# Performance work log

Measured on AMD Instinct MI355X. Metric: run time of the kernel, lower is better.

## Reference

```python
import jax, jax.numpy as jnp
import numpy as np
from jax import lax

DN = ('NCHW', 'OIHW', 'NCHW')


def conv2d(x, w, b, stride, pad):
    y = lax.conv_general_dilated(x, w, (stride, stride), [(pad, pad), (pad, pad)],
                                 dimension_numbers=DN)
    return y + b[None, :, None, None]


def conv_transpose2d_k4s2p1(x, w, b):
    # torch ConvTranspose2d(k=4, s=2, p=1); w is torch layout [Cin, Cout, 4, 4].
    # Equivalent forward conv: lhs_dilation=2, pad = k-1-p = 2, spatially-flipped kernel.
    k = jnp.flip(w, (2, 3)).transpose(1, 0, 2, 3)  # -> OIHW [Cout, Cin, 4, 4]
    y = lax.conv_general_dilated(x, k, (1, 1), [(2, 2), (2, 2)],
                                 lhs_dilation=(2, 2), dimension_numbers=DN)
    return y + b[None, :, None, None]


def setup_inputs() -> dict:
    key = jax.random.key(0)
    ks = jax.random.split(key, 16)

    def w(k, shape):
        fan_in = int(np.prod(shape[1:]))
        return jax.random.normal(k, shape, jnp.float32) * np.float32(1.0 / np.sqrt(fan_in))

    inp = {}
    inp['x'] = jax.random.uniform(ks[0], (256, 1, 128, 128), jnp.float32)
    # Encoder
    inp['enc_w1'] = w(ks[1], (32, 1, 4, 4));   inp['enc_b1'] = jnp.zeros((32,), jnp.float32)
    inp['enc_w2'] = w(ks[2], (64, 32, 4, 4));  inp['enc_b2'] = jnp.zeros((64,), jnp.float32)
    inp['enc_w3'] = w(ks[3], (64, 64, 3, 3));  inp['enc_b3'] = jnp.zeros((64,), jnp.float32)
    inp['enc_w4'] = w(ks[4], (32, 64, 1, 1));  inp['enc_b4'] = jnp.zeros((32,), jnp.float32)
    # Codebook: uniform(-sqrt(3/512), sqrt(3/512))
    mx = np.float32(np.sqrt(3.0 / 512.0))
    inp['codebook'] = jax.random.uniform(ks[5], (512, 32), jnp.float32, -mx, mx)
    # Decoder
    inp['dec_w1'] = w(ks[6], (64, 32, 3, 3));  inp['dec_b1'] = jnp.zeros((64,), jnp.float32)
    inp['dect_w1'] = w(ks[7], (64, 32, 4, 4)); inp['dect_b1'] = jnp.zeros((32,), jnp.float32)  # torch [Cin,Cout,k,k]
    inp['dect_w2'] = w(ks[8], (32, 1, 4, 4));  inp['dect_b2'] = jnp.zeros((1,), jnp.float32)
    return inp


def vqvae_forward(x, enc_w1, enc_b1, enc_w2, enc_b2, enc_w3, enc_b3, enc_w4, enc_b4,
                  codebook, dec_w1, dec_b1, dect_w1, dect_b1, dect_w2, dect_b2):
    # Encoder: 128 -> 64 -> 32 spatial, 32 channels out
    h = jax.nn.relu(conv2d(x, enc_w1, enc_b1, 2, 1))
    h = jax.nn.relu(conv2d(h, enc_w2, enc_b2, 2, 1))
    h = jax.nn.relu(conv2d(h, enc_w3, enc_b3, 1, 1))
    z = conv2d(h, enc_w4, enc_b4, 1, 0)            # [B, 32, 32, 32]

    # Vector quantization (NCHW -> NHWC -> flat)
    zin = jnp.moveaxis(z, 1, -1)                   # [B, H, W, D]
    flat = zin.reshape(-1, zin.shape[-1])          # [N, D]
    dists = (jnp.sum(flat * flat, -1, keepdims=True)
             + jnp.sum(codebook * codebook, -1)
             - 2.0 * flat @ codebook.T)            # [N, K]
    idx = jnp.argmin(dists, -1)                    # [N]
    quant = codebook[idx].reshape(zin.shape)       # == one_hot @ codebook

    emb_loss = jnp.mean((quant - lax.stop_gradient(zin)) ** 2)
    com_loss = 0.26 * jnp.mean((lax.stop_gradient(quant) - zin) ** 2)
    vq_loss = emb_loss + com_loss
    quant = zin + lax.stop_gradient(quant - zin)   # straight-through
    qz = jnp.moveaxis(quant, -1, 1)                # [B, 32, 32, 32]

    # Decoder: 32 -> 64 -> 128 spatial
    d = jax.nn.relu(conv2d(qz, dec_w1, dec_b1, 1, 1))
    d = jax.nn.relu(conv_transpose2d_k4s2p1(d, dect_w1, dect_b1))
    recon = jax.nn.sigmoid(conv_transpose2d_k4s2p1(d, dect_w2, dect_b2))
    return recon, vq_loss


def reference(x, enc_w1, enc_b1, enc_w2, enc_b2, enc_w3, enc_b3, enc_w4, enc_b4,
              codebook, dec_w1, dec_b1, dect_w1, dect_b1, dect_w2, dect_b2):
    return vqvae_forward(x, enc_w1, enc_b1, enc_w2, enc_b2, enc_w3, enc_b3, enc_w4, enc_b4,
                         codebook, dec_w1, dec_b1, dect_w1, dect_b1, dect_w2, dect_b2)
```

## Files before the change

kernel.cpp:

```cpp
#include <hip/hip_runtime.h>
#include <math.h>

typedef __attribute__((ext_vector_type(8))) short short8;
typedef __attribute__((ext_vector_type(4))) float f32x4;

__device__ inline unsigned short f2bf(float f) {
  unsigned u = __float_as_uint(f);
  u = (u + 0x7fffu + ((u >> 16) & 1u)) >> 16;
  return (unsigned short)u;
}

__global__ __launch_bounds__(256, 4)
void conv1_lds(const float* __restrict__ x, const float* __restrict__ w,
               const float* __restrict__ bias, float* __restrict__ out) {
  int bid = blockIdx.x;
  int cchunk = bid & 1;
  int t4 = (bid >> 1) & 3;
  int n = bid >> 3;
  int co0 = cchunk * 16;
  int y0 = t4 * 16;
  int yi0 = 2 * y0 - 1;

  __shared__ float xs[34 * 128];
  __shared__ float wl[16][16];

  int t = threadIdx.x;
  for (int idx = t; idx < 34 * 128; idx += 256) {
    int gy = yi0 + (idx >> 7);
    int gx = idx & 127;
    bool ok = (unsigned)gy < 128;
    xs[idx] = ok ? x[(size_t)n * 16384 + gy * 128 + gx] : 0.f;
  }
  {
    int cc = t & 15;
    int tap = t >> 4;
    if (t < 256) wl[tap][cc] = w[(size_t)(co0 + cc) * 16 + tap];
  }
  __syncthreads();

  int sx = t & 63;
  int rg = t >> 6;

  float acc[4][16];
#pragma unroll
  for (int j = 0; j < 4; j++)
#pragma unroll
    for (int c = 0; c < 16; c++) acc[j][c] = 0.f;

  int ix0 = 2 * sx - 1;
#pragma unroll
  for (int ky = 0; ky < 4; ky++) {
#pragma unroll
    for (int kx = 0; kx < 4; kx++) {
      int ix = ix0 + kx;
      bool xok = (unsigned)ix < 128;
      float xv[4];
#pragma unroll
      for (int j = 0; j < 4; j++) {
        int lrow = 2 * (4 * rg + j) + ky;
        float v = xs[lrow * 128 + (xok ? ix : 0)];
        xv[j] = xok ? v : 0.f;
      }
      const float* wr = &wl[ky * 4 + kx][0];
#pragma unroll
      for (int c = 0; c < 16; c += 4) {
        float4 wv = *(const float4*)(wr + c);
#pragma unroll
        for (int j = 0; j < 4; j++) {
          acc[j][c + 0] = fmaf(xv[j], wv.x, acc[j][c + 0]);
          acc[j][c + 1] = fmaf(xv[j], wv.y, acc[j][c + 1]);
          acc[j][c + 2] = fmaf(xv[j], wv.z, acc[j][c + 2]);
          acc[j][c + 3] = fmaf(xv[j], wv.w, acc[j][c + 3]);
        }
      }
    }
  }

#pragma unroll
  for (int j = 0; j < 4; j++) {
    int oy = y0 + 4 * rg + j;
    float* op = out + (((size_t)n * 32 + co0) * 64 + oy) * 64 + sx;
#pragma unroll
    for (int c = 0; c < 16; c++) {
      float v = acc[j][c] + bias[co0 + c];
      op[(size_t)c * 4096] = fmaxf(v, 0.f);
    }
  }
}

template<int CIN, int COUT, int CCH>
__global__ __launch_bounds__(256, 4)
void conv4x4s2_h4(const float* __restrict__ x, const float* __restrict__ w,
                  const float* __restrict__ bias, float* __restrict__ out) {
  constexpr int NCH = COUT / CCH;
  int bid = blockIdx.x;
  int cchunk = bid % NCH;
  int n = bid / NCH;
  int co0 = cchunk * CCH;

  __shared__ float xs[66 * 64];
  __shared__ float wl[16][CCH];

  int t = threadIdx.x;
  int sx = t & 31;
  int sy0 = t >> 5;
  int ix0 = 2 * sx - 1;

  if (t < 128) {
    int r = (t >> 6) ? 65 : 0;
    xs[r * 64 + (t & 63)] = 0.f;
  }

  float acc[4][CCH];
#pragma unroll
  for (int j = 0; j < 4; j++)
#pragma unroll
    for (int c = 0; c < CCH; c++) acc[j][c] = 0.f;

  const float* xn = x + (size_t)n * CIN * 4096;

  for (int ci = 0; ci < CIN; ci++) {
    __syncthreads();
#pragma unroll
    for (int k = 0; k < 4; k++) {
      int idx = k * 1024 + t * 4;
      int row = idx >> 6;
      int col = idx & 63;
      *(float4*)(xs + (row + 1) * 64 + col) =
          *(const float4*)(xn + (size_t)ci * 4096 + idx);
    }
    {
      int cc = t & (CCH - 1);
      int tap = t >> 4;
      if (tap < 16) wl[tap][cc] = w[(size_t)(co0 + cc) * (CIN * 16) + ci * 16 + tap];
    }
    __syncthreads();

#pragma unroll
    for (int ky = 0; ky < 4; ky++) {
#pragma unroll
      for (int kx = 0; kx < 4; kx++) {
        int ix = ix0 + kx;
        bool xok = (unsigned)ix < 64;
        int ixs = xok ? ix : 0;
        float xv[4];
#pragma unroll
        for (int j = 0; j < 4; j++) {
          int row = 2 * (sy0 + j * 8) + ky;
          float v = xs[row * 64 + ixs];
          xv[j] = xok ? v : 0.f;
        }
        const float* wr = &wl[ky * 4 + kx][0];
#pragma unroll
        for (int c = 0; c < CCH; c += 4) {
          float4 wv = *(const float4*)(wr + c);
#pragma unroll
          for (int j = 0; j < 4; j++) {
            acc[j][c + 0] = fmaf(xv[j], wv.x, acc[j][c + 0]);
            acc[j][c + 1] = fmaf(xv[j], wv.y, acc[j][c + 1]);
            acc[j][c + 2] = fmaf(xv[j], wv.z, acc[j][c + 2]);
            acc[j][c + 3] = fmaf(xv[j], wv.w, acc[j][c + 3]);
          }
        }
      }
    }
  }

#pragma unroll
  for (int j = 0; j < 4; j++) {
    int sy = sy0 + j * 8;
    float* op = out + (((size_t)n * COUT + co0) * 32 + sy) * 32 + sx;
#pragma unroll
    for (int c = 0; c < CCH; c++) {
      float v = acc[j][c] + bias[co0 + c];
      v = fmaxf(v, 0.f);
      op[(size_t)c * 1024] = v;
    }
  }
}

template<int CIN, int COUT, int CCH>
__global__ __launch_bounds__(256, 4)
void conv3x3_h4(const float* __restrict__ x, const float* __restrict__ w,
                const float* __restrict__ bias, float* __restrict__ out) {
  constexpr int NCH = COUT / CCH;
  int bid = blockIdx.x;
  int cchunk = bid % NCH;
  int n = bid / NCH;
  int co0 = cchunk * CCH;

  __shared__ float xs[4][34 * 32];
  __shared__ float wl[4 * 9][CCH];

  int t = threadIdx.x;
  int sx = t & 31;
  int rg = t >> 5;

  {
    int p = t >> 6;
    int idx = t & 63;
    int row = (idx >> 5) ? 33 : 0;
    xs[p][row * 32 + (idx & 31)] = 0.f;
  }

  float acc[4][CCH];
#pragma unroll
  for (int j = 0; j < 4; j++)
#pragma unroll
    for (int c = 0; c < CCH; c++) acc[j][c] = 0.f;

  const float* xn = x + (size_t)n * CIN * 1024;

  for (int cg = 0; cg < CIN / 4; cg++) {
    __syncthreads();
#pragma unroll
    for (int k = 0; k < 4; k++) {
      int row = t >> 3;
      int col = (t & 7) * 4;
      *(float4*)(&xs[k][(row + 1) * 32 + col]) =
          *(const float4*)(xn + (size_t)(cg * 4 + k) * 1024 + t * 4);
    }
    for (int i = t; i < 4 * 9 * CCH; i += 256) {
      int cc = i % CCH;
      int row = i / CCH;
      int c4 = row / 9, kk = row % 9;
      wl[row][cc] = w[(size_t)(co0 + cc) * (CIN * 9) + (cg * 4 + c4) * 9 + kk];
    }
    __syncthreads();

#pragma unroll
    for (int c4 = 0; c4 < 4; c4++) {
      const float* xc = &xs[c4][0];
      float xv[6][3];
#pragma unroll
      for (int cx = 0; cx < 3; cx++) {
        int ix = sx - 1 + cx;
        bool xok = (unsigned)ix < 32;
        int ixs = xok ? ix : 0;
#pragma unroll
        for (int r = 0; r < 6; r++) {
          float v = xc[(4 * rg + r) * 32 + ixs];
          xv[r][cx] = xok ? v : 0.f;
        }
      }
#pragma unroll
      for (int ky = 0; ky < 3; ky++) {
#pragma unroll
        for (int kx = 0; kx < 3; kx++) {
          const float* wr = &wl[c4 * 9 + ky * 3 + kx][0];
#pragma unroll
          for (int c = 0; c < CCH; c += 4) {
            float4 wv = *(const float4*)(wr + c);
#pragma unroll
            for (int j = 0; j < 4; j++) {
              float xx = xv[j + ky][kx];
              acc[j][c + 0] = fmaf(xx, wv.x, acc[j][c + 0]);
              acc[j][c + 1] = fmaf(xx, wv.y, acc[j][c + 1]);
              acc[j][c + 2] = fmaf(xx, wv.z, acc[j][c + 2]);
              acc[j][c + 3] = fmaf(xx, wv.w, acc[j][c + 3]);
            }
          }
        }
      }
    }
  }

#pragma unroll
  for (int j = 0; j < 4; j++) {
    int sy = 4 * rg + j;
    float* op = out + (((size_t)n * COUT + co0) * 32 + sy) * 32 + sx;
#pragma unroll
    for (int c = 0; c < CCH; c++) {
      float v = acc[j][c] + bias[co0 + c];
      v = fmaxf(v, 0.f);
      op[(size_t)c * 1024] = v;
    }
  }
}

__global__ void wprep_dect1(const float* __restrict__ tw1,
                            unsigned short* __restrict__ Bws) {
  int i = blockIdx.x * 256 + threadIdx.x;
  if (i < 32768) {
    int ci = i & 63;
    int co = (i >> 6) & 31;
    int tap = (i >> 11) & 3;
    int par = i >> 13;
    int py = par >> 1, px = par & 1;
    int ky0 = (py + 1) & 1, kx0 = (px + 1) & 1;
    int kyi = tap >> 1, kxi = tap & 1;
    int ky = ky0 + 2 * kyi, kx = kx0 + 2 * kxi;
    Bws[i] = f2bf(tw1[(((size_t)ci * 32 + co) * 4 + ky) * 4 + kx]);
  }
}

__global__ void wprep_dec1(const float* __restrict__ dw1,
                           unsigned short* __restrict__ Wd1) {
  int i = blockIdx.x * 256 + threadIdx.x;
  if (i < 18432) {
    int ci = i & 31;
    int tap = (i >> 5) % 9;
    int co = i / 288;
    Wd1[i] = f2bf(dw1[(size_t)(co * 32 + ci) * 9 + tap]);
  }
}

__global__ __launch_bounds__(256, 4)
void dec1_mfma(const float* __restrict__ qz,
               const unsigned short* __restrict__ Wd1,
               const float* __restrict__ bias, float* __restrict__ d1) {
  int strip = blockIdx.x & 3;
  int smp = blockIdx.x >> 2;
  int y0 = strip * 8;

  __shared__ __align__(16) unsigned short xt[10 * 34 * 32];

  int t = threadIdx.x;
  for (int idx = t; idx < 16 * 10 * 34; idx += 256) {
    int cc = idx % 34;
    int tmp = idx / 34;
    int rr = tmp % 10;
    int pp = tmp / 10;
    int gy = y0 - 1 + rr;
    int gx = cc - 1;
    bool ok = ((unsigned)gy < 32) && ((unsigned)gx < 32);
    const float* p = qz + ((size_t)smp * 32 + 2 * pp) * 1024 + gy * 32 + gx;
    float v0 = ok ? p[0] : 0.f;
    float v1 = ok ? p[1024] : 0.f;
    unsigned pk = (unsigned)f2bf(v0) | ((unsigned)f2bf(v1) << 16);
    *(unsigned*)(&xt[(rr * 34 + cc) * 32 + 2 * pp]) = pk;
  }

  int lane = t & 63;
  int wv = t >> 6;
  int mlo = lane & 15;
  int khi = lane >> 4;

  short8 afr[9];
#pragma unroll
  for (int tap = 0; tap < 9; tap++)
    afr[tap] = *(const short8*)(Wd1 + (size_t)(wv * 16 + mlo) * 288 +
                                tap * 32 + khi * 8);
  float bb[4];
#pragma unroll
  for (int r = 0; r < 4; r++) bb[r] = bias[wv * 16 + khi * 4 + r];

  __syncthreads();

  for (int pt = 0; pt < 16; pt++) {
    int rl = pt >> 1;
    int chf = pt & 1;
    f32x4 acc = {0.f, 0.f, 0.f, 0.f};
#pragma unroll
    for (int tap = 0; tap < 9; tap++) {
      int ky = tap / 3, kx = tap % 3;
      const unsigned short* bp =
          xt + (((rl + ky) * 34) + chf * 16 + mlo + kx) * 32 + khi * 8;
      short8 b = *(const short8*)bp;
      acc = __builtin_amdgcn_mfma_f32_16x16x32_bf16(afr[tap], b, acc, 0, 0, 0);
    }
    int gyo = y0 + rl;
    int gxo = chf * 16 + mlo;
#pragma unroll
    for (int r = 0; r < 4; r++) {
      int co = wv * 16 + khi * 4 + r;
      d1[(((size_t)smp * 64 + co) * 32 + gyo) * 32 + gxo] =
          fmaxf(acc[r] + bb[r], 0.f);
    }
  }
}

__global__ __launch_bounds__(256, 4)
void convt_mfma(const float* __restrict__ d1,
                const unsigned short* __restrict__ Bws,
                const float* __restrict__ bias, float* __restrict__ d2) {
  constexpr int CP = 72;
  int bid = blockIdx.x;
  int rp = bid & 15;
  int smp = bid >> 4;

  __shared__ __align__(16) unsigned short xt[4 * 34 * CP];

  int t = threadIdx.x;

  for (int idx = t; idx < 32 * 4 * 34; idx += 256) {
    int cc = idx % 34;
    int tmp = idx / 34;
    int rr = tmp & 3;
    int pp = tmp >> 2;
    int gy = 2 * rp - 1 + rr;
    int gx = cc - 1;
    bool ok = ((unsigned)gy < 32) && ((unsigned)gx < 32);
    const float* p = d1 + ((size_t)smp * 64 + 2 * pp) * 1024 + gy * 32 + gx;
    float v0 = ok ? p[0] : 0.f;
    float v1 = ok ? p[1024] : 0.f;
    unsigned pk = (unsigned)f2bf(v0) | ((unsigned)f2bf(v1) << 16);
    *(unsigned*)(&xt[(rr * 34 + cc) * CP + 2 * pp]) = pk;
  }
  __syncthreads();

  int lane = t & 63;
  int wv = t >> 6;
  int row2 = wv >> 1;
  int c0 = (wv & 1) * 16;
  int mlo = lane & 15;
  int khi = lane >> 4;

  f32x4 acc[4][2];
#pragma unroll
  for (int par = 0; par < 4; par++)
#pragma unroll
    for (int nt = 0; nt < 2; nt++) {
      f32x4 z = {0.f, 0.f, 0.f, 0.f};
      acc[par][nt] = z;
    }

#pragma unroll
  for (int par = 0; par < 4; par++) {
    int py = par >> 1, px = par & 1;
    int ky0 = (py + 1) & 1, kx0 = (px + 1) & 1;
    int ay = (py + 1 - ky0) >> 1;
    int ax = (px + 1 - kx0) >> 1;
#pragma unroll
    for (int tap = 0; tap < 4; tap++) {
      int kyi = tap >> 1, kxi = tap & 1;
      int rrp = row2 + 1 + (ay - kyi);
      int ccb = c0 + 1 + (ax - kxi);
#pragma unroll
      for (int kc = 0; kc < 2; kc++) {
        const unsigned short* ap =
            xt + ((rrp * 34) + ccb + mlo) * CP + kc * 32 + khi * 8;
        short8 a = *(const short8*)ap;
#pragma unroll
        for (int nt = 0; nt < 2; nt++) {
          const unsigned short* bp =
              Bws + (((size_t)(par * 4 + tap) * 32 + nt * 16 + mlo) * 64) +
              kc * 32 + khi * 8;
          short8 b = *(const short8*)bp;
          acc[par][nt] =
              __builtin_amdgcn_mfma_f32_16x16x32_bf16(a, b, acc[par][nt], 0, 0, 0);
        }
      }
    }
  }

  int sy = 2 * rp + row2;
#pragma unroll
  for (int par = 0; par < 4; par++) {
    int py = par >> 1, px = par & 1;
    int oy = 2 * sy + py;
#pragma unroll
    for (int nt = 0; nt < 2; nt++) {
      int co = nt * 16 + mlo;
      float b = bias[co];
      float* op = d2 + (((size_t)smp * 32 + co) * 64 + oy) * 64;
#pragma unroll
      for (int r = 0; r < 4; r++) {
        int sx = c0 + khi * 4 + r;
        int ox = 2 * sx + px;
        op[ox] = fmaxf(acc[par][nt][r] + b, 0.f);
      }
    }
  }
}

__global__ __launch_bounds__(256, 4)
void dect2_full(const float* __restrict__ x, const float* __restrict__ w,
                const float* __restrict__ bias, float* __restrict__ out) {
  int ptile = blockIdx.x & 3;
  int n = blockIdx.x >> 2;
  int y0 = ptile * 16;

  __shared__ float xs[8][1152];
  int t = threadIdx.x;
  int sx = t & 63;
  int r4 = t >> 6;

  float acc[4][4];
#pragma unroll
  for (int j = 0; j < 4; j++)
#pragma unroll
    for (int p = 0; p < 4; p++) acc[j][p] = 0.f;

  const float* xn = x + (size_t)n * 32 * 4096;

  for (int cg = 0; cg < 4; cg++) {
    __syncthreads();
    for (int idx = t; idx < 8 * 1152; idx += 256) {
      int ch = idx / 1152;
      int rem = idx % 1152;
      int iy = y0 - 1 + rem / 64;
      int ix = rem & 63;
      bool ok = (unsigned)iy < 64;
      xs[ch][rem] = ok ? xn[(size_t)(cg * 8 + ch) * 4096 + iy * 64 + ix] : 0.f;
    }
    __syncthreads();

#pragma unroll
    for (int c4 = 0; c4 < 8; c4++) {
      int ci = cg * 8 + c4;
      const float* xc = &xs[c4][0];
      float xv[6][3];
#pragma unroll
      for (int r = 0; r < 6; r++) {
        int srow = 4 * r4 + r;
#pragma unroll
        for (int cx = 0; cx < 3; cx++) {
          int ix = sx - 1 + cx;
          bool ok = (unsigned)ix < 64;
          float v = xc[ok ? srow * 64 + ix : 0];
          xv[r][cx] = ok ? v : 0.f;
        }
      }
      float w16[16];
#pragma unroll
      for (int q = 0; q < 4; q++) {
        float4 ww = *(const float4*)(w + ci * 16 + 4 * q);
        w16[4 * q + 0] = ww.x; w16[4 * q + 1] = ww.y;
        w16[4 * q + 2] = ww.z; w16[4 * q + 3] = ww.w;
      }
#pragma unroll
      for (int py = 0; py < 2; py++) {
#pragma unroll
        for (int px = 0; px < 2; px++) {
          int par = py * 2 + px;
          int ky0 = (py + 1) & 1, kx0 = (px + 1) & 1;
          int ay = (py + 1 - ky0) >> 1;
          int ax = (px + 1 - kx0) >> 1;
#pragma unroll
          for (int kyi = 0; kyi < 2; kyi++) {
#pragma unroll
            for (int kxi = 0; kxi < 2; kxi++) {
              float wv = w16[(ky0 + 2 * kyi) * 4 + (kx0 + 2 * kxi)];
#pragma unroll
              for (int j = 0; j < 4; j++) {
                float xx = xv[j + ay + 1 - kyi][ax + 1 - kxi];
                acc[j][par] = fmaf(xx, wv, acc[j][par]);
              }
            }
          }
        }
      }
    }
  }

  float b0 = bias[0];
#pragma unroll
  for (int j = 0; j < 4; j++) {
    int iy = y0 + 4 * r4 + j;
#pragma unroll
    for (int py = 0; py < 2; py++) {
      float v0 = acc[j][py * 2 + 0] + b0;
      float v1 = acc[j][py * 2 + 1] + b0;
      float2 o;
      o.x = 1.f / (1.f + expf(-v0));
      o.y = 1.f / (1.f + expf(-v1));
      int oy = 2 * iy + py;
      *(float2*)(out + (size_t)n * 16384 + oy * 128 + 2 * sx) = o;
    }
  }
}

__global__ void cbn_prep(const float* __restrict__ cb, float* __restrict__ cbn) {
#pragma clang fp contract(off)
  int k = blockIdx.x * 256 + threadIdx.x;
  if (k < 512) {
    float m[32];
#pragma unroll
    for (int d = 0; d < 32; d++) {
      float c = cb[k * 32 + d];
      m[d] = c * c;
    }
    float r[8];
#pragma unroll
    for (int j = 0; j < 8; j++)
      r[j] = ((m[j] + m[8 + j]) + m[16 + j]) + m[24 + j];
    cbn[k] = ((r[0] + r[1]) + (r[2] + r[3])) + ((r[4] + r[5]) + (r[6] + r[7]));
  }
}

__global__ __launch_bounds__(256)
void vq_fused(const float* __restrict__ h3, const float* __restrict__ w4,
              const float* __restrict__ b4, const float* __restrict__ cb,
              const float* __restrict__ cbn, float* __restrict__ qz,
              float* __restrict__ loss) {
  __shared__ float wl[64][32];
  int tid = threadIdx.x;
  for (int i = tid; i < 2048; i += 256) {
    int co = i & 31;
    int ci = i >> 5;
    wl[ci][co] = w4[(size_t)co * 64 + ci];
  }
  __syncthreads();

  int n = blockIdx.x >> 2;
  int p = (blockIdx.x & 3) * 256 + tid;
  const float* hn = h3 + (size_t)n * 65536;

  float zv[32];
#pragma unroll
  for (int c = 0; c < 32; c++) zv[c] = 0.f;
  for (int ci = 0; ci < 64; ci++) {
    float xv = hn[(size_t)ci * 1024 + p];
#pragma unroll
    for (int c = 0; c < 32; c += 4) {
      float4 wv = *(const float4*)&wl[ci][c];
      zv[c + 0] = fmaf(xv, wv.x, zv[c + 0]);
      zv[c + 1] = fmaf(xv, wv.y, zv[c + 1]);
      zv[c + 2] = fmaf(xv, wv.z, zv[c + 2]);
      zv[c + 3] = fmaf(xv, wv.w, zv[c + 3]);
    }
  }
#pragma unroll
  for (int c = 0; c < 32; c++) zv[c] = zv[c] + b4[c];

  float zz;
  {
#pragma clang fp contract(off)
    float m[32];
#pragma unroll
    for (int d = 0; d < 32; d++) m[d] = zv[d] * zv[d];
    float r[8];
#pragma unroll
    for (int j = 0; j < 8; j++)
      r[j] = ((m[j] + m[8 + j]) + m[16 + j]) + m[24 + j];
    zz = ((r[0] + r[1]) + (r[2] + r[3])) + ((r[4] + r[5]) + (r[6] + r[7]));
  }

  float best = 3.4e38f;
  int bk = 0;
  for (int k4 = 0; k4 < 512; k4 += 4) {
    float4 cn = *(const float4*)(cbn + k4);
    float da[4];
#pragma unroll
    for (int u = 0; u < 4; u++) da[u] = 0.f;
#pragma unroll
    for (int d = 0; d < 32; d += 4) {
#pragma unroll
      for (int u = 0; u < 4; u++) {
        float4 c = *(const float4*)(cb + (size_t)(k4 + u) * 32 + d);
        float a = da[u];
        a = fmaf(zv[d + 0], c.x, a);
        a = fmaf(zv[d + 1], c.y, a);
        a = fmaf(zv[d + 2], c.z, a);
        a = fmaf(zv[d + 3], c.w, a);
        da[u] = a;
      }
    }
#pragma unroll
    for (int u = 0; u < 4; u++) {
      float cnu = (u == 0) ? cn.x : (u == 1) ? cn.y : (u == 2) ? cn.z : cn.w;
      float s;
      {
#pragma clang fp contract(off)
        s = (zz + cnu) - 2.f * da[u];
      }
      int k = k4 + u;
      if (s < best) { best = s; bk = k; }
    }
  }

  float lsum = 0.f;
  float* qn = qz + (size_t)n * 32768;
#pragma unroll
  for (int d = 0; d < 32; d += 4) {
#pragma clang fp contract(off)
    float4 q = *(const float4*)(cb + (size_t)bk * 32 + d);
    float e;
    e = q.x - zv[d + 0]; lsum = fmaf(e, e, lsum);
    e = q.y - zv[d + 1]; lsum = fmaf(e, e, lsum);
    e = q.z - zv[d + 2]; lsum = fmaf(e, e, lsum);
    e = q.w - zv[d + 3]; lsum = fmaf(e, e, lsum);
    qn[(size_t)(d + 0) * 1024 + p] = zv[d + 0] + (q.x - zv[d + 0]);
    qn[(size_t)(d + 1) * 1024 + p] = zv[d + 1] + (q.y - zv[d + 1]);
    qn[(size_t)(d + 2) * 1024 + p] = zv[d + 2] + (q.z - zv[d + 2]);
    qn[(size_t)(d + 3) * 1024 + p] = zv[d + 3] + (q.w - zv[d + 3]);
  }

#pragma unroll
  for (int off = 32; off; off >>= 1) lsum += __shfl_down(lsum, off, 64);
  if ((tid & 63) == 0) atomicAdd(loss, lsum);
}

__global__ void finalize_loss(const float* __restrict__ loss, float* __restrict__ out) {
  if (threadIdx.x == 0) {
    float m = loss[0] / 8388608.f;
    out[0] = m + 0.26f * m;
  }
}

extern "C" void kernel_launch(void* const* d_in, const int* in_sizes, int n_in,
                              void* d_out, int out_size, void* d_ws, size_t ws_size,
                              hipStream_t stream) {
  (void)in_sizes; (void)n_in; (void)out_size;
  const float* x   = (const float*)d_in[0];
  const float* ew1 = (const float*)d_in[1];
  const float* eb1 = (const float*)d_in[2];
  const float* ew2 = (const float*)d_in[3];
  const float* eb2 = (const float*)d_in[4];
  const float* ew3 = (const float*)d_in[5];
  const float* eb3 = (const float*)d_in[6];
  const float* ew4 = (const float*)d_in[7];
  const float* eb4 = (const float*)d_in[8];
  const float* cb  = (const float*)d_in[9];
  const float* dw1 = (const float*)d_in[10];
  const float* db1 = (const float*)d_in[11];
  const float* tw1 = (const float*)d_in[12];
  const float* tb1 = (const float*)d_in[13];
  const float* tw2 = (const float*)d_in[14];
  const float* tb2 = (const float*)d_in[15];
  float* out = (float*)d_out;

  auto need = [](size_t c) -> size_t {
    return (c * 196608 + 516 + 16384 + 9216) * 4;
  };
  int nchunks = 4;
  if (ws_size >= need(256)) nchunks = 1;
  else if (ws_size >= need(128)) nchunks = 2;
  int chunk = 256 / nchunks;

  float* ws = (float*)d_ws;
  float* A = ws;
  float* B = A + (size_t)chunk * 131072;
  float* cbn = B + (size_t)chunk * 65536;
  float* lossacc = cbn + 512;
  unsigned short* Bws = (unsigned short*)(cbn + 516);
  unsigned short* Wd1 = (unsigned short*)(cbn + 516 + 16384);

  float* h1 = A;
  float* h2 = B;
  float* h3 = A;
  float* qz = A + (size_t)chunk * 98304;
  float* d1 = B;
  float* d2 = A;

  cbn_prep<<<2, 256, 0, stream>>>(cb, cbn);
  wprep_dect1<<<128, 256, 0, stream>>>(tw1, Bws);
  wprep_dec1<<<72, 256, 0, stream>>>(dw1, Wd1);
  (void)hipMemsetAsync(lossacc, 0, 4, stream);

  for (int c = 0; c < nchunks; c++) {
    const float* xc = x + (size_t)c * chunk * 128 * 128;
    float* outc = out + (size_t)c * chunk * 128 * 128;

    conv1_lds<<<chunk * 8, 256, 0, stream>>>(xc, ew1, eb1, h1);
    conv4x4s2_h4<32, 64, 16>
        <<<chunk * 4, 256, 0, stream>>>(h1, ew2, eb2, h2);
    conv3x3_h4<64, 64, 16>
        <<<chunk * 4, 256, 0, stream>>>(h2, ew3, eb3, h3);

    vq_fused<<<chunk * 4, 256, 0, stream>>>(h3, ew4, eb4, cb, cbn, qz, lossacc);

    dec1_mfma<<<chunk * 4, 256, 0, stream>>>(qz, Wd1, db1, d1);
    convt_mfma<<<chunk * 16, 256, 0, stream>>>(d1, Bws, tb1, d2);
    dect2_full<<<chunk * 4, 256, 0, stream>>>(d2, tw2, tb2, outc);
  }

  finalize_loss<<<1, 64, 0, stream>>>(lossacc, out + 4194304);
}
```

Before: 1.084 ms.

## Use padded parity-split LDS layouts and 8x8 register tiles in encoder convs

```diff
diff --git a/kernel.cpp b/kernel.cpp
--- a/kernel.cpp
+++ b/kernel.cpp
@@ -90,26 +90,22 @@
 
 template<int CIN, int COUT, int CCH>
 __global__ __launch_bounds__(256, 4)
-void conv4x4s2_h4(const float* __restrict__ x, const float* __restrict__ w,
-                  const float* __restrict__ bias, float* __restrict__ out) {
+void conv4x4s2_p(const float* __restrict__ x, const float* __restrict__ w,
+                 const float* __restrict__ bias, float* __restrict__ out) {
   constexpr int NCH = COUT / CCH;
   int bid = blockIdx.x;
   int cchunk = bid % NCH;
   int n = bid / NCH;
   int co0 = cchunk * CCH;
 
-  __shared__ float xs[66 * 64];
+  __shared__ float xs[66 * 68];
   __shared__ float wl[16][CCH];
 
   int t = threadIdx.x;
   int sx = t & 31;
   int sy0 = t >> 5;
-  int ix0 = 2 * sx - 1;
-
-  if (t < 128) {
-    int r = (t >> 6) ? 65 : 0;
-    xs[r * 64 + (t & 63)] = 0.f;
-  }
+
+  for (int i = t; i < 66 * 68; i += 256) xs[i] = 0.f;
 
   float acc[4][CCH];
 #pragma unroll
@@ -126,8 +122,13 @@
       int idx = k * 1024 + t * 4;
       int row = idx >> 6;
       int col = idx & 63;
-      *(float4*)(xs + (row + 1) * 64 + col) =
-          *(const float4*)(xn + (size_t)ci * 4096 + idx);
+      float4 v = *(const float4*)(xn + (size_t)ci * 4096 + idx);
+      float* rp = xs + (row + 1) * 68;
+      int h = col >> 1;
+      rp[34 + h]     = v.x;
+      rp[h + 1]      = v.y;
+      rp[34 + h + 1] = v.z;
+      rp[h + 2]      = v.w;
     }
     {
       int cc = t & (CCH - 1);
@@ -140,15 +141,12 @@
     for (int ky = 0; ky < 4; ky++) {
 #pragma unroll
       for (int kx = 0; kx < 4; kx++) {
-        int ix = ix0 + kx;
-        bool xok = (unsigned)ix < 64;
-        int ixs = xok ? ix : 0;
+        int pc = ((kx & 1) ? 34 : 0) + sx + (kx >> 1);
         float xv[4];
 #pragma unroll
         for (int j = 0; j < 4; j++) {
           int row = 2 * (sy0 + j * 8) + ky;
-          float v = xs[row * 64 + ixs];
-          xv[j] = xok ? v : 0.f;
+          xv[j] = xs[row * 68 + pc];
         }
         const float* wr = &wl[ky * 4 + kx][0];
 #pragma unroll
@@ -179,35 +177,31 @@
   }
 }
 
-template<int CIN, int COUT, int CCH>
-__global__ __launch_bounds__(256, 4)
-void conv3x3_h4(const float* __restrict__ x, const float* __restrict__ w,
+template<int CIN, int COUT>
+__global__ __launch_bounds__(256, 3)
+void conv3x3_r8(const float* __restrict__ x, const float* __restrict__ w,
                 const float* __restrict__ bias, float* __restrict__ out) {
-  constexpr int NCH = COUT / CCH;
+  constexpr int NCH = COUT / 16;
   int bid = blockIdx.x;
   int cchunk = bid % NCH;
   int n = bid / NCH;
-  int co0 = cchunk * CCH;
-
-  __shared__ float xs[4][34 * 32];
-  __shared__ float wl[4 * 9][CCH];
+  int co0 = cchunk * 16;
+
+  __shared__ float xs[4 * 34 * 34];
+  __shared__ float wl[4 * 9][16];
 
   int t = threadIdx.x;
   int sx = t & 31;
-  int rg = t >> 5;
-
-  {
-    int p = t >> 6;
-    int idx = t & 63;
-    int row = (idx >> 5) ? 33 : 0;
-    xs[p][row * 32 + (idx & 31)] = 0.f;
-  }
-
-  float acc[4][CCH];
-#pragma unroll
-  for (int j = 0; j < 4; j++)
-#pragma unroll
-    for (int c = 0; c < CCH; c++) acc[j][c] = 0.f;
+  int rg = (t >> 5) & 3;
+  int cob = (t >> 7) * 8;
+
+  for (int i = t; i < 4 * 34 * 34; i += 256) xs[i] = 0.f;
+
+  float acc[8][8];
+#pragma unroll
+  for (int j = 0; j < 8; j++)
+#pragma unroll
+    for (int c = 0; c < 8; c++) acc[j][c] = 0.f;
 
   const float* xn = x + (size_t)n * CIN * 1024;
 
@@ -217,12 +211,13 @@
     for (int k = 0; k < 4; k++) {
       int row = t >> 3;
       int col = (t & 7) * 4;
-      *(float4*)(&xs[k][(row + 1) * 32 + col]) =
-          *(const float4*)(xn + (size_t)(cg * 4 + k) * 1024 + t * 4);
-    }
-    for (int i = t; i < 4 * 9 * CCH; i += 256) {
-      int cc = i % CCH;
-      int row = i / CCH;
+      float4 v = *(const float4*)(xn + (size_t)(cg * 4 + k) * 1024 + t * 4);
+      float* dst = xs + k * 1156 + (row + 1) * 34 + col + 1;
+      dst[0] = v.x; dst[1] = v.y; dst[2] = v.z; dst[3] = v.w;
+    }
+    for (int i = t; i < 4 * 9 * 16; i += 256) {
+      int cc = i & 15;
+      int row = i >> 4;
       int c4 = row / 9, kk = row % 9;
       wl[row][cc] = w[(size_t)(co0 + cc) * (CIN * 9) + (cg * 4 + c4) * 9 + kk];
     }
@@ -230,35 +225,32 @@
 
 #pragma unroll
     for (int c4 = 0; c4 < 4; c4++) {
-      const float* xc = &xs[c4][0];
-      float xv[6][3];
-#pragma unroll
-      for (int cx = 0; cx < 3; cx++) {
-        int ix = sx - 1 + cx;
-        bool xok = (unsigned)ix < 32;
-        int ixs = xok ? ix : 0;
-#pragma unroll
-        for (int r = 0; r < 6; r++) {
-          float v = xc[(4 * rg + r) * 32 + ixs];
-          xv[r][cx] = xok ? v : 0.f;
-        }
+      const float* xc = xs + c4 * 1156;
+      float xv[10][3];
+#pragma unroll
+      for (int r = 0; r < 10; r++) {
+#pragma unroll
+        for (int cx = 0; cx < 3; cx++)
+          xv[r][cx] = xc[(8 * rg + r) * 34 + sx + cx];
       }
 #pragma unroll
       for (int ky = 0; ky < 3; ky++) {
 #pragma unroll
         for (int kx = 0; kx < 3; kx++) {
-          const float* wr = &wl[c4 * 9 + ky * 3 + kx][0];
-#pragma unroll
-          for (int c = 0; c < CCH; c += 4) {
-            float4 wv = *(const float4*)(wr + c);
-#pragma unroll
-            for (int j = 0; j < 4; j++) {
-              float xx = xv[j + ky][kx];
-              acc[j][c + 0] = fmaf(xx, wv.x, acc[j][c + 0]);
-              acc[j][c + 1] = fmaf(xx, wv.y, acc[j][c + 1]);
-              acc[j][c + 2] = fmaf(xx, wv.z, acc[j][c + 2]);
-              acc[j][c + 3] = fmaf(xx, wv.w, acc[j][c + 3]);
-            }
+          const float* wr = &wl[c4 * 9 + ky * 3 + kx][cob];
+          float4 w0 = *(const float4*)(wr);
+          float4 w1 = *(const float4*)(wr + 4);
+#pragma unroll
+          for (int j = 0; j < 8; j++) {
+            float xx = xv[j + ky][kx];
+            acc[j][0] = fmaf(xx, w0.x, acc[j][0]);
+            acc[j][1] = fmaf(xx, w0.y, acc[j][1]);
+            acc[j][2] = fmaf(xx, w0.z, acc[j][2]);
+            acc[j][3] = fmaf(xx, w0.w, acc[j][3]);
+            acc[j][4] = fmaf(xx, w1.x, acc[j][4]);
+            acc[j][5] = fmaf(xx, w1.y, acc[j][5]);
+            acc[j][6] = fmaf(xx, w1.z, acc[j][6]);
+            acc[j][7] = fmaf(xx, w1.w, acc[j][7]);
           }
         }
       }
@@ -266,12 +258,12 @@
   }
 
 #pragma unroll
-  for (int j = 0; j < 4; j++) {
-    int sy = 4 * rg + j;
-    float* op = out + (((size_t)n * COUT + co0) * 32 + sy) * 32 + sx;
-#pragma unroll
-    for (int c = 0; c < CCH; c++) {
-      float v = acc[j][c] + bias[co0 + c];
+  for (int j = 0; j < 8; j++) {
+    int sy = 8 * rg + j;
+    float* op = out + (((size_t)n * COUT + co0 + cob) * 32 + sy) * 32 + sx;
+#pragma unroll
+    for (int c = 0; c < 8; c++) {
+      float v = acc[j][c] + bias[co0 + cob + c];
       v = fmaxf(v, 0.f);
       op[(size_t)c * 1024] = v;
     }
@@ -744,9 +736,9 @@
     float* outc = out + (size_t)c * chunk * 128 * 128;
 
     conv1_lds<<<chunk * 8, 256, 0, stream>>>(xc, ew1, eb1, h1);
-    conv4x4s2_h4<32, 64, 16>
+    conv4x4s2_p<32, 64, 16>
         <<<chunk * 4, 256, 0, stream>>>(h1, ew2, eb2, h2);
-    conv3x3_h4<64, 64, 16>
+    conv3x3_r8<64, 64>
         <<<chunk * 4, 256, 0, stream>>>(h2, ew3, eb3, h3);
 
     vq_fused<<<chunk * 4, 256, 0, stream>>>(h3, ew4, eb4, cb, cbn, qz, lossacc);
```

After: 1.039 ms, median of 3. 4.2% less time.
